# Optimization experiments

Hardware: AMD Instinct MI355X
Metric: run time of the kernel (lower is better)

Reference implementation:

```python
import jax, jax.numpy as jnp
import numpy as np

EPS = 1e-9
LDIM = 4  # dim_g + dim_t + dim_b + dim_w


def _mvn_logpdf(v, F):
    # batched zero-mean multivariate normal log-density, v: (N,O), F: (N,O,O)
    chol = jnp.linalg.cholesky(F)
    z = jax.scipy.linalg.solve_triangular(chol, v[..., None], lower=True)[..., 0]
    quad = jnp.sum(z * z, axis=-1)
    logdet = 2.0 * jnp.sum(jnp.log(jnp.diagonal(chol, axis1=-2, axis2=-1)), axis=-1)
    k = v.shape[-1]
    return -0.5 * (quad + logdet + k * jnp.log(2.0 * jnp.pi))


def _forward(y, B_G, B_T, B_B, B_W, lambda_r1_free, lambda_r2_free,
             q_diag, r_diag, gamma1, gamma2_learnable):
    N, Nt, O = y.shape
    L = LDIM
    # ----- _build_matrices -----
    B11 = jnp.zeros((L, L)).at[0, 0].set(B_G[0, 0]).at[1, 1].set(B_T[0, 0]).at[2, 2].set(B_B[0, 0])
    B22 = jnp.zeros((L, L)).at[3, 3].set(B_W[0, 0])
    B12 = jnp.zeros((L, L)).at[3, :3].set(1.0 / 3.0)  # regime1 factors feed shared factor
    B21 = jnp.zeros((L, L))
    L1 = jnp.zeros((O, L))
    L1 = L1.at[0, 0].set(1.0).at[1, 0].set(lambda_r1_free[0]).at[2, 0].set(lambda_r1_free[1])
    L1 = L1.at[3, 1].set(1.0).at[4, 1].set(lambda_r1_free[2]).at[5, 1].set(lambda_r1_free[3])
    L1 = L1.at[6, 2].set(1.0).at[7, 2].set(lambda_r1_free[4]).at[8, 2].set(lambda_r1_free[5])
    L2 = jnp.zeros((O, L)).at[0, 3].set(1.0).at[1:, 3].set(lambda_r2_free)
    Q = jnp.diag(jnp.abs(q_diag) + 1e-4)
    R = jnp.diag(jnp.abs(r_diag) + 1e-4)
    F_JIT = 1e-5 * jnp.eye(O)
    I_L = jnp.eye(L)
    P22_CONST = 0.9999

    # ----- initial beliefs ('informative') -----
    prob0 = jnp.tile(jnp.array([0.99, 0.01], jnp.float32), (N, 1))
    eta0 = jnp.zeros((N, L), y.dtype)
    P0 = jnp.tile(jnp.diag(jnp.array([1000.0, 1000.0, 1000.0, 1e-9], y.dtype))[None], (N, 1, 1))

    def predict(B, eta, P):
        # eta: (N,L), P: (N,L,L)
        return eta @ B.T, jnp.einsum('ij,njk,lk->nil', B, P, B) + Q

    def innov(Lm, e, Pp, y_t):
        v = y_t - e @ Lm.T
        F = jnp.einsum('oi,nij,pj->nop', Lm, Pp, Lm) + R + F_JIT
        return v, F

    def kupdate(e, Pp, Lm, v, F):
        LP = jnp.einsum('oi,nij->noj', Lm, Pp)          # (N,O,L)
        K = jnp.swapaxes(jnp.linalg.solve(F, LP), -1, -2)  # P Lm^T F^{-1}, (N,L,O)
        e_u = e + jnp.einsum('nlo,no->nl', K, v)
        IKL = I_L - K @ Lm                                # (N,L,L)
        P_u = IKL @ Pp @ jnp.swapaxes(IKL, -1, -2) + jnp.einsum('nlo,op,nmp->nlm', K, R, K)
        return e_u, P_u

    def collapse(w_a, w_b, e_a, e_b, P_a, P_b):
        e = w_a[:, None] * e_a + w_b[:, None] * e_b
        da, db = e_a - e, e_b - e
        P = (w_a[:, None, None] * (P_a + da[:, :, None] * da[:, None, :])
             + w_b[:, None, None] * (P_b + db[:, :, None] * db[:, None, :]))
        return e, P

    def step(carry, y_t):
        prob, eta1, eta2, P1, P2, ll = carry
        # HMM transition: p11 depends on regime-1 state (first L-1 components)
        logit_p11 = gamma1 + eta1[:, :3] @ gamma2_learnable
        p11 = jax.nn.sigmoid(logit_p11)
        # predictions for the 4 regime transitions (origin -> destination)
        e11, Pp11 = predict(B11, eta1, P1)
        e12, Pp12 = predict(B21, eta2, P2)
        e21, Pp21 = predict(B12, eta1, P1)
        e22, Pp22 = predict(B22, eta2, P2)
        v11, F11 = innov(L1, e11, Pp11, y_t)
        v12, F12 = innov(L1, e12, Pp12, y_t)
        v21, F21 = innov(L2, e21, Pp21, y_t)
        v22, F22 = innov(L2, e22, Pp22, y_t)
        ll11 = _mvn_logpdf(v11, F11)
        ll12 = _mvn_logpdf(v12, F12)
        ll21 = _mvn_logpdf(v21, F21)
        ll22 = _mvn_logpdf(v22, F22)
        lp = jnp.log(prob + EPS)
        c11 = lp[:, 0] + jnp.log(p11 + EPS) + ll11
        c12 = lp[:, 1] + np.log(1.0 - P22_CONST + EPS) + ll12
        c21 = lp[:, 0] + jnp.log(1.0 - p11 + EPS) + ll21
        c22 = lp[:, 1] + np.log(P22_CONST + EPS) + ll22
        logp = jnp.stack([c11, c12, c21, c22], axis=1)
        ll_t = jax.scipy.special.logsumexp(logp, axis=1)
        pt = jnp.exp(logp - ll_t[:, None])
        pr1 = pt[:, 0] + pt[:, 1]
        pr2 = pt[:, 2] + pt[:, 3]
        W11 = pt[:, 0] / (pr1 + EPS)
        W12 = pt[:, 1] / (pr1 + EPS)
        W21 = pt[:, 2] / (pr2 + EPS)
        W22 = pt[:, 3] / (pr2 + EPS)
        eu11, Pu11 = kupdate(e11, Pp11, L1, v11, F11)
        eu12, Pu12 = kupdate(e12, Pp12, L1, v12, F12)
        eu21, Pu21 = kupdate(e21, Pp21, L2, v21, F21)
        eu22, Pu22 = kupdate(e22, Pp22, L2, v22, F22)
        eta1n, P1n = collapse(W11, W12, eu11, eu12, Pu11, Pu12)
        eta2n, P2n = collapse(W21, W22, eu21, eu22, Pu21, Pu22)
        probn = jnp.stack([pr1, pr2], axis=1)
        return (probn, eta1n, eta2n, P1n, P2n, ll + ll_t.sum()), None

    carry0 = (prob0, eta0, eta0, P0, P0, jnp.zeros((), y.dtype))
    (_, _, _, _, _, total_ll), _ = jax.lax.scan(step, carry0, jnp.swapaxes(y, 0, 1))
    return total_ll


def setup_inputs() -> dict:
    key = jax.random.key(0)
    ks = jax.random.split(key, 12)
    N, Nt, O = 16384, 64, 9
    f32 = jnp.float32
    return {
        'y': jax.random.normal(ks[0], (N, Nt, O), f32),
        'B_G': jax.random.uniform(ks[1], (1, 1), f32, 0.6, 0.95),  # Beta(5,1.5)-like AR coeffs
        'B_T': jax.random.uniform(ks[2], (1, 1), f32, 0.6, 0.95),
        'B_B': jax.random.uniform(ks[3], (1, 1), f32, 0.6, 0.95),
        'B_W': jax.random.uniform(ks[4], (1, 1), f32, 0.6, 0.95),
        'lambda_r1_free': jax.random.normal(ks[5], (6,), f32),
        'lambda_r2_free': jax.random.normal(ks[6], (O - 1,), f32),
        'q_diag': jax.random.uniform(ks[7], (LDIM,), f32),
        'r_diag': jax.random.uniform(ks[8], (O,), f32),
        'gamma1': jnp.abs(jax.random.normal(ks[9], (), f32)),
        'gamma2_learnable': jax.random.normal(ks[10], (LDIM - 1,), f32),
    }


def reference(y, B_G, B_T, B_B, B_W, lambda_r1_free, lambda_r2_free,
              q_diag, r_diag, gamma1, gamma2_learnable):
    return _forward(y, B_G, B_T, B_B, B_W, lambda_r1_free, lambda_r2_free,
                    q_diag, r_diag, gamma1, gamma2_learnable)
```

## Files before the change

kernel.cpp:

```cpp
#include <hip/hip_runtime.h>


typedef float v2f __attribute__((ext_vector_type(2)));
typedef v2f v2fu __attribute__((aligned(4)));

static __device__ __forceinline__ float frcp(float x)  { return __builtin_amdgcn_rcpf(x); }
static __device__ __forceinline__ float frsq(float x)  { return __builtin_amdgcn_rsqf(x); }
static __device__ __forceinline__ float fexp2(float x) { return __builtin_amdgcn_exp2f(x); }
static __device__ __forceinline__ float flog2(float x) { return __builtin_amdgcn_logf(x); }
static __device__ __forceinline__ v2f sp(float x) { return (v2f){x, x}; }
static __device__ __forceinline__ v2f rsq2(v2f a) { return (v2f){frsq(a.x), frsq(a.y)}; }

#define EPSF   1e-9f
#define L2E    1.4426950408889634f
#define LN2    0.6931471805599453f
#define L2_2PI_9 23.86346461225016f
#define C12F   1.00001e-4f
#define P22F   0.99990001f
#define QK     (-0.5f * L2E)

__global__ __launch_bounds__(64, 1)
void kf_kernel(const float* __restrict__ y,
               const float* __restrict__ pBG, const float* __restrict__ pBT,
               const float* __restrict__ pBB, const float* __restrict__ pBW,
               const float* __restrict__ lam1, const float* __restrict__ lam2,
               const float* __restrict__ qd,  const float* __restrict__ rd,
               const float* __restrict__ pG1, const float* __restrict__ pG2,
               float* __restrict__ partial, int N, int Nt)
{
    const int lane = threadIdx.x;
    const int sid  = blockIdx.x * 64 + lane;
    const bool valid = (sid < N);
    const int rowlen = Nt * 9;

    const float bg = pBG[0], bt = pBT[0], bb = pBB[0], bw = pBW[0];
    const float a1 = lam1[0], a2 = lam1[1];
    const float a4 = lam1[2], a5 = lam1[3];
    const float a7 = lam1[4], a8 = lam1[5];
    float l2v[9], id[9], ld[9];
    l2v[0] = 1.f;
    #pragma unroll
    for (int i = 0; i < 8; ++i) l2v[i + 1] = lam2[i];
    float l2detD = 0.f;
    #pragma unroll
    for (int o = 0; o < 9; ++o) {
        float dv = fabsf(rd[o]) + 1.0e-4f + 1.0e-5f;
        id[o] = 1.0f / dv;
        ld[o] = l2v[o] * id[o];
        l2detD += flog2(dv);
    }
    const float id8 = id[8], ld8 = ld[8];
    const v2f idv01 = {id[0], id[1]}, idv23 = {id[2], id[3]},
              idv45 = {id[4], id[5]}, idv67 = {id[6], id[7]};
    const v2f ldv01 = {ld[0], ld[1]}, ldv23 = {ld[2], ld[3]},
              ldv45 = {ld[4], ld[5]}, ldv67 = {ld[6], ld[7]};
    const float aid0 = id[0],    aid1 = a1*id[1], aid2 = a2*id[2];
    const float aid3 = id[3],    aid4 = a4*id[4], aid5 = a5*id[5];
    const float aid6 = id[6],    aid7 = a7*id[7], aid8 = a8*id[8];
    const float q0 = fabsf(qd[0]) + 1e-4f, q1 = fabsf(qd[1]) + 1e-4f;
    const float q2 = fabsf(qd[2]) + 1e-4f, q3 = fabsf(qd[3]) + 1e-4f;
    const float g0 = id[0] + a1*a1*id[1] + a2*a2*id[2];
    const float g1 = id[3] + a4*a4*id[4] + a5*a5*id[5];
    const float g2 = id[6] + a7*a7*id[7] + a8*a8*id[8];
    float h = 0.f;
    #pragma unroll
    for (int o = 0; o < 9; ++o) h += l2v[o] * ld[o];
    const float pk0 = q0 / (1.f + q0 * g0);
    const float pk1 = q1 / (1.f + q1 * g1);
    const float pk2 = q2 / (1.f + q2 * g2);
    const float C12D = C12F * frsq((1.f + q0*g0) * (1.f + q1*g1) * (1.f + q2*g2));
    const float gam1 = pG1[0], w0c = pG2[0], w1c = pG2[1], w2c = pG2[2];
    const float CC = -0.5f * (l2detD + L2_2PI_9);
    const float bg2 = bg*bg, bt2 = bt*bt, bb2 = bb*bb, bw2 = bw*bw;
    const float bgbt = bg*bt, bgbb = bg*bb, btbb = bt*bb;
    const v2f hv = {h, h};

    float pf1 = 0.99f + EPSF, pf2 = 0.01f + EPSF;
    float se0 = 0.f, se1 = 0.f, se2 = 0.f;
    float p00 = 1000.f, p01 = 0.f, p02 = 0.f, p11 = 1000.f, p12 = 0.f, p22 = 1000.f;
    float sm2 = 0.f, sp2 = 1e-9f;
    float acc2 = 0.f;

    struct Yr { v2f ab, cd, ef, gh; float i8; };
    struct YB { float uy0, uy1, uy2, yl, ydy, f0, f1, f2, q12e; };

    const char* rowb = (const char*)(y + (size_t)(valid ? sid : 0) * rowlen);
    auto loadY = [&](Yr& r, int t) {
        const char* p = rowb + t * 36;
        r.ab = *(const v2fu*)(p);
        r.cd = *(const v2fu*)(p + 8);
        r.ef = *(const v2fu*)(p + 16);
        r.gh = *(const v2fu*)(p + 24);
        r.i8 = *(const float*)(p + 32);
    };
    auto computeYB = [&](const Yr& r) {
        YB o;
        v2f m0 = idv01*r.ab, m1 = idv23*r.cd, m2 = idv45*r.ef, m3 = idv67*r.gh;
        v2f yq = m0*r.ab + m1*r.cd + m2*r.ef + m3*r.gh;
        o.ydy = fmaf(id8*r.i8, r.i8, yq.x + yq.y);
        v2f la = ldv01*r.ab + ldv23*r.cd + ldv45*r.ef + ldv67*r.gh;
        o.yl = fmaf(ld8, r.i8, la.x + la.y);
        o.uy0 = fmaf(aid2, r.cd.x, fmaf(aid1, r.ab.y, aid0*r.ab.x));
        o.uy1 = fmaf(aid5, r.ef.y, fmaf(aid4, r.ef.x, aid3*r.cd.y));
        o.uy2 = fmaf(aid8, r.i8,   fmaf(aid7, r.gh.y, aid6*r.gh.x));
        o.f0 = pk0*o.uy0; o.f1 = pk1*o.uy1; o.f2 = pk2*o.uy2;
        o.q12e = QK * (o.ydy - (o.f0*o.uy0 + o.f1*o.uy1 + o.f2*o.uy2));
        return o;
    };

    auto step = [&](const YB& yb) {
        float logit = fmaf(w2c, se2, fmaf(w1c, se1, fmaf(w0c, se0, gam1)));
        float p11s = frcp(1.f + fexp2(-L2E * logit));
        float pp1 = pf1 * (p11s + EPSF);
        float pp2 = pf1 * (1.f - p11s + EPSF);

        float e0 = bg*se0, e1 = bt*se1, e2 = bb*se2;
        float s00 = fmaf(bg2, p00, q0), s11 = fmaf(bt2, p11, q1), s22 = fmaf(bb2, p22, q2);
        float s01 = bgbt*p01, s02 = bgbb*p02, s12 = btbb*p12;

        float u0 = fmaf(-g0, e0, yb.uy0);
        float u1 = fmaf(-g1, e1, yb.uy1);
        float u2 = fmaf(-g2, e2, yb.uy2);
        float vdv = yb.ydy - (e0*(yb.uy0+u0) + e1*(yb.uy1+u1) + e2*(yb.uy2+u2));

        float m00 = fmaf(s00, g0, 1.f), m11 = fmaf(s11, g1, 1.f), m22 = fmaf(s22, g2, 1.f);
        float m01 = s01*g1, m02 = s02*g2;
        float m10 = s01*g0, m20 = s02*g0;
        float m12 = s12*g2, m21 = s12*g1;
        float c00 = fmaf(m11, m22, -m12*m21);
        float c01 = fmaf(m12, m20, -m10*m22);
        float c02 = fmaf(m10, m21, -m11*m20);
        float c10 = fmaf(m02, m21, -m01*m22);
        float c11 = fmaf(m00, m22, -m02*m20);
        float c12 = fmaf(m01, m20, -m00*m21);
        float c20 = fmaf(m01, m12, -m02*m11);
        float c21 = fmaf(m02, m10, -m00*m12);
        float c22 = fmaf(m00, m11, -m01*m10);
        float det = fmaf(m02, c02, fmaf(m01, c01, m00*c00));
        float rs  = frsq(det);
        float iM  = rs * rs;
        float SC00 = fmaf(s02, c20, fmaf(s01, c10, s00*c00));
        float SC01 = fmaf(s02, c21, fmaf(s01, c11, s00*c01));
        float SC02 = fmaf(s02, c22, fmaf(s01, c12, s00*c02));
        float SC11 = fmaf(s12, c21, fmaf(s11, c11, s01*c01));
        float SC12 = fmaf(s12, c22, fmaf(s11, c12, s01*c02));
        float SC22 = fmaf(s22, c22, fmaf(s12, c12, s02*c02));

        float n0 = fmaf(SC02, u2, fmaf(SC01, u1, SC00*u0));
        float n1 = fmaf(SC12, u2, fmaf(SC11, u1, SC01*u0));
        float n2 = fmaf(SC22, u2, fmaf(SC12, u1, SC02*u0));
        float un = fmaf(u2, n2, fmaf(u1, n1, u0*n0));
        float quad11 = fmaf(-iM, un, vdv);
        float eu0 = fmaf(iM, n0, e0), eu1 = fmaf(iM, n1, e1), eu2 = fmaf(iM, n2, e2);

        float seS = se0 + se1 + se2;
        float sPs = fmaf(2.f, (p01 + p02) + p12, (p00 + p11) + p22);
        v2f m2v; m2v.x = seS * (1.f/3.f);          m2v.y = bw * sm2;
        v2f pvv; pvv.x = fmaf(sPs, 1.f/9.f, q3);   pvv.y = fmaf(bw2, sp2, q3);
        v2f ylv = sp(yb.yl);
        v2f u1v = ylv - m2v*hv;
        v2f vdav = sp(yb.ydy) - m2v*(sp(2.f*yb.yl) - m2v*hv);
        v2f denv = sp(1.f) + pvv*hv;
        v2f rv  = rsq2(denv);
        v2f puv = pvv*(rv*rv);
        v2f pu1 = puv*u1v;
        v2f quadv = vdav - pu1*u1v;
        v2f euv = m2v + pu1;

        float q11e = QK*quad11;
        float q21e = QK*quadv.x, q22e = QK*quadv.y;
        float Mq = fmaxf(fmaxf(q11e, yb.q12e), fmaxf(q21e, q22e));
        float w11 = pp1*rs        * fexp2(q11e - Mq);
        float w12 = pf2*C12D      * fexp2(yb.q12e - Mq);
        float w21 = pp2*rv.x      * fexp2(q21e - Mq);
        float w22 = pf2*P22F*rv.y * fexp2(q22e - Mq);
        float pr1n = w11 + w12, pr2n = w21 + w22;
        float ssum = pr1n + pr2n;
        acc2 += Mq + flog2(ssum);
        float inv1 = frcp(fmaf(EPSF, ssum, pr1n));
        float inv2 = frcp(fmaf(EPSF, ssum, pr2n));
        float issum = frcp(ssum);
        float W11 = w11*inv1, W12 = w12*inv1;
        float W21 = w21*inv2, W22 = w22*inv2;
        pf1 = fmaf(pr1n, issum, EPSF);
        pf2 = fmaf(pr2n, issum, EPSF);
        float W11i = W11 * iM;

        float ne0 = fmaf(W12, yb.f0, W11*eu0);
        float ne1 = fmaf(W12, yb.f1, W11*eu1);
        float ne2 = fmaf(W12, yb.f2, W11*eu2);
        float da0 = eu0-ne0, da1 = eu1-ne1, da2 = eu2-ne2;
        float db0 = yb.f0-ne0, db1 = yb.f1-ne1, db2 = yb.f2-ne2;
        p00 = fmaf(W12, fmaf(db0, db0, pk0), fmaf(W11, da0*da0, W11i*SC00));
        p01 = fmaf(W12, db0*db1,             fmaf(W11, da0*da1, W11i*SC01));
        p02 = fmaf(W12, db0*db2,             fmaf(W11, da0*da2, W11i*SC02));
        p11 = fmaf(W12, fmaf(db1, db1, pk1), fmaf(W11, da1*da1, W11i*SC11));
        p12 = fmaf(W12, db1*db2,             fmaf(W11, da1*da2, W11i*SC12));
        p22 = fmaf(W12, fmaf(db2, db2, pk2), fmaf(W11, da2*da2, W11i*SC22));
        se0 = ne0; se1 = ne1; se2 = ne2;

        float nm2 = fmaf(W22, euv.y, W21*euv.x);
        v2f dcv = euv - sp(nm2);
        v2f tv = puv + dcv*dcv;
        sp2 = fmaf(W22, tv.y, W21*tv.x);
        sm2 = nm2;
    };

    Yr A, B; YB ya, yb;
    loadY(A, 0);
    loadY(B, 1);
    ya = computeYB(A);
    for (int t = 0; t < Nt; t += 2) {
        step(ya);
        yb = computeYB(B);
        if (t + 2 < Nt) loadY(A, t + 2);
        step(yb);
        if (t + 2 < Nt) ya = computeYB(A);
        if (t + 3 < Nt) loadY(B, t + 3);
    }

    float acc = valid ? (acc2 + (float)Nt * CC) * LN2 : 0.f;
    #pragma unroll
    for (int off = 32; off; off >>= 1) acc += __shfl_down(acc, off, 64);
    if (lane == 0) partial[blockIdx.x] = acc;
}

__global__ __launch_bounds__(64)
void reduce_k(const float* __restrict__ part, float* __restrict__ out, int nb)
{
    float s = 0.f;
    for (int i = threadIdx.x; i < nb; i += 64) s += part[i];
    #pragma unroll
    for (int off = 32; off; off >>= 1) s += __shfl_down(s, off, 64);
    if (threadIdx.x == 0) out[0] = s;
}

extern "C" void kernel_launch(void* const* d_in, const int* in_sizes, int n_in,
                              void* d_out, int out_size, void* d_ws, size_t ws_size,
                              hipStream_t stream)
{
    const float* y    = (const float*)d_in[0];
    const float* pBG  = (const float*)d_in[1];
    const float* pBT  = (const float*)d_in[2];
    const float* pBB  = (const float*)d_in[3];
    const float* pBW  = (const float*)d_in[4];
    const float* lam1 = (const float*)d_in[5];
    const float* lam2 = (const float*)d_in[6];
    const float* qd   = (const float*)d_in[7];
    const float* rd   = (const float*)d_in[8];
    const float* pG1  = (const float*)d_in[9];
    const float* pG2  = (const float*)d_in[10];

    const int total = in_sizes[0];
    const int Nt = 64, O = 9;
    const int N = total / (Nt * O);
    const int blocks = (N + 63) / 64;

    float* partial = (float*)d_ws;
    kf_kernel<<<blocks, 64, 0, stream>>>(y, pBG, pBT, pBB, pBW, lam1, lam2,
                                         qd, rd, pG1, pG2, partial, N, Nt);
    reduce_k<<<1, 64, 0, stream>>>(partial, (float*)d_out, blocks);
}
```

Before: 127.6 us.

## Interleave two independent series per thread to raise instruction-level parallelism

```diff
diff --git a/kernel.cpp b/kernel.cpp
--- a/kernel.cpp
+++ b/kernel.cpp
@@ -29,8 +29,10 @@
                float* __restrict__ partial, int N, int Nt)
 {
     const int lane = threadIdx.x;
-    const int sid  = blockIdx.x * 64 + lane;
-    const bool valid = (sid < N);
+    const int base = blockIdx.x * 128;
+    const int sidA = base + lane;
+    const int sidB = base + 64 + lane;
+    const bool vA = (sidA < N), vB = (sidB < N);
     const int rowlen = Nt * 9;
 
     const float bg = pBG[0], bt = pBT[0], bb = pBB[0], bw = pBW[0];
@@ -75,17 +77,28 @@
     const float bgbt = bg*bt, bgbb = bg*bb, btbb = bt*bb;
     const v2f hv = {h, h};
 
-    float pf1 = 0.99f + EPSF, pf2 = 0.01f + EPSF;
-    float se0 = 0.f, se1 = 0.f, se2 = 0.f;
-    float p00 = 1000.f, p01 = 0.f, p02 = 0.f, p11 = 1000.f, p12 = 0.f, p22 = 1000.f;
-    float sm2 = 0.f, sp2 = 1e-9f;
-    float acc2 = 0.f;
+    struct St {
+        float pf1, pf2;
+        float se0, se1, se2;
+        float p00, p01, p02, p11, p12, p22;
+        float sm2, sp2, acc2;
+    };
+    auto initSt = [&](St& s) {
+        s.pf1 = 0.99f + EPSF; s.pf2 = 0.01f + EPSF;
+        s.se0 = 0.f; s.se1 = 0.f; s.se2 = 0.f;
+        s.p00 = 1000.f; s.p01 = 0.f; s.p02 = 0.f;
+        s.p11 = 1000.f; s.p12 = 0.f; s.p22 = 1000.f;
+        s.sm2 = 0.f; s.sp2 = 1e-9f; s.acc2 = 0.f;
+    };
+    St st0, st1;
+    initSt(st0); initSt(st1);
 
     struct Yr { v2f ab, cd, ef, gh; float i8; };
     struct YB { float uy0, uy1, uy2, yl, ydy, f0, f1, f2, q12e; };
 
-    const char* rowb = (const char*)(y + (size_t)(valid ? sid : 0) * rowlen);
-    auto loadY = [&](Yr& r, int t) {
+    const char* row0 = (const char*)(y + (size_t)(vA ? sidA : 0) * rowlen);
+    const char* row1 = (const char*)(y + (size_t)(vB ? sidB : 0) * rowlen);
+    auto loadY = [&](Yr& r, const char* rowb, int t) {
         const char* p = rowb + t * 36;
         r.ab = *(const v2fu*)(p);
         r.cd = *(const v2fu*)(p + 8);
@@ -108,15 +121,15 @@
         return o;
     };
 
-    auto step = [&](const YB& yb) {
-        float logit = fmaf(w2c, se2, fmaf(w1c, se1, fmaf(w0c, se0, gam1)));
+    auto step = [&](St& st, const YB& yb) {
+        float logit = fmaf(w2c, st.se2, fmaf(w1c, st.se1, fmaf(w0c, st.se0, gam1)));
         float p11s = frcp(1.f + fexp2(-L2E * logit));
-        float pp1 = pf1 * (p11s + EPSF);
-        float pp2 = pf1 * (1.f - p11s + EPSF);
-
-        float e0 = bg*se0, e1 = bt*se1, e2 = bb*se2;
-        float s00 = fmaf(bg2, p00, q0), s11 = fmaf(bt2, p11, q1), s22 = fmaf(bb2, p22, q2);
-        float s01 = bgbt*p01, s02 = bgbb*p02, s12 = btbb*p12;
+        float pp1 = st.pf1 * (p11s + EPSF);
+        float pp2 = st.pf1 * (1.f - p11s + EPSF);
+
+        float e0 = bg*st.se0, e1 = bt*st.se1, e2 = bb*st.se2;
+        float s00 = fmaf(bg2, st.p00, q0), s11 = fmaf(bt2, st.p11, q1), s22 = fmaf(bb2, st.p22, q2);
+        float s01 = bgbt*st.p01, s02 = bgbb*st.p02, s12 = btbb*st.p12;
 
         float u0 = fmaf(-g0, e0, yb.uy0);
         float u1 = fmaf(-g1, e1, yb.uy1);
@@ -153,10 +166,10 @@
         float quad11 = fmaf(-iM, un, vdv);
         float eu0 = fmaf(iM, n0, e0), eu1 = fmaf(iM, n1, e1), eu2 = fmaf(iM, n2, e2);
 
-        float seS = se0 + se1 + se2;
-        float sPs = fmaf(2.f, (p01 + p02) + p12, (p00 + p11) + p22);
-        v2f m2v; m2v.x = seS * (1.f/3.f);          m2v.y = bw * sm2;
-        v2f pvv; pvv.x = fmaf(sPs, 1.f/9.f, q3);   pvv.y = fmaf(bw2, sp2, q3);
+        float seS = st.se0 + st.se1 + st.se2;
+        float sPs = fmaf(2.f, (st.p01 + st.p02) + st.p12, (st.p00 + st.p11) + st.p22);
+        v2f m2v; m2v.x = seS * (1.f/3.f);          m2v.y = bw * st.sm2;
+        v2f pvv; pvv.x = fmaf(sPs, 1.f/9.f, q3);   pvv.y = fmaf(bw2, st.sp2, q3);
         v2f ylv = sp(yb.yl);
         v2f u1v = ylv - m2v*hv;
         v2f vdav = sp(yb.ydy) - m2v*(sp(2.f*yb.yl) - m2v*hv);
@@ -170,20 +183,20 @@
         float q11e = QK*quad11;
         float q21e = QK*quadv.x, q22e = QK*quadv.y;
         float Mq = fmaxf(fmaxf(q11e, yb.q12e), fmaxf(q21e, q22e));
-        float w11 = pp1*rs        * fexp2(q11e - Mq);
-        float w12 = pf2*C12D      * fexp2(yb.q12e - Mq);
-        float w21 = pp2*rv.x      * fexp2(q21e - Mq);
-        float w22 = pf2*P22F*rv.y * fexp2(q22e - Mq);
+        float w11 = pp1*rs           * fexp2(q11e - Mq);
+        float w12 = st.pf2*C12D      * fexp2(yb.q12e - Mq);
+        float w21 = pp2*rv.x         * fexp2(q21e - Mq);
+        float w22 = st.pf2*P22F*rv.y * fexp2(q22e - Mq);
         float pr1n = w11 + w12, pr2n = w21 + w22;
         float ssum = pr1n + pr2n;
-        acc2 += Mq + flog2(ssum);
+        st.acc2 += Mq + flog2(ssum);
         float inv1 = frcp(fmaf(EPSF, ssum, pr1n));
         float inv2 = frcp(fmaf(EPSF, ssum, pr2n));
         float issum = frcp(ssum);
         float W11 = w11*inv1, W12 = w12*inv1;
         float W21 = w21*inv2, W22 = w22*inv2;
-        pf1 = fmaf(pr1n, issum, EPSF);
-        pf2 = fmaf(pr2n, issum, EPSF);
+        st.pf1 = fmaf(pr1n, issum, EPSF);
+        st.pf2 = fmaf(pr2n, issum, EPSF);
         float W11i = W11 * iM;
 
         float ne0 = fmaf(W12, yb.f0, W11*eu0);
@@ -191,35 +204,39 @@
         float ne2 = fmaf(W12, yb.f2, W11*eu2);
         float da0 = eu0-ne0, da1 = eu1-ne1, da2 = eu2-ne2;
         float db0 = yb.f0-ne0, db1 = yb.f1-ne1, db2 = yb.f2-ne2;
-        p00 = fmaf(W12, fmaf(db0, db0, pk0), fmaf(W11, da0*da0, W11i*SC00));
-        p01 = fmaf(W12, db0*db1,             fmaf(W11, da0*da1, W11i*SC01));
-        p02 = fmaf(W12, db0*db2,             fmaf(W11, da0*da2, W11i*SC02));
-        p11 = fmaf(W12, fmaf(db1, db1, pk1), fmaf(W11, da1*da1, W11i*SC11));
-        p12 = fmaf(W12, db1*db2,             fmaf(W11, da1*da2, W11i*SC12));
-        p22 = fmaf(W12, fmaf(db2, db2, pk2), fmaf(W11, da2*da2, W11i*SC22));
-        se0 = ne0; se1 = ne1; se2 = ne2;
+        st.p00 = fmaf(W12, fmaf(db0, db0, pk0), fmaf(W11, da0*da0, W11i*SC00));
+        st.p01 = fmaf(W12, db0*db1,             fmaf(W11, da0*da1, W11i*SC01));
+        st.p02 = fmaf(W12, db0*db2,             fmaf(W11, da0*da2, W11i*SC02));
+        st.p11 = fmaf(W12, fmaf(db1, db1, pk1), fmaf(W11, da1*da1, W11i*SC11));
+        st.p12 = fmaf(W12, db1*db2,             fmaf(W11, da1*da2, W11i*SC12));
+        st.p22 = fmaf(W12, fmaf(db2, db2, pk2), fmaf(W11, da2*da2, W11i*SC22));
+        st.se0 = ne0; st.se1 = ne1; st.se2 = ne2;
 
         float nm2 = fmaf(W22, euv.y, W21*euv.x);
         v2f dcv = euv - sp(nm2);
         v2f tv = puv + dcv*dcv;
-        sp2 = fmaf(W22, tv.y, W21*tv.x);
-        sm2 = nm2;
-    };
-
-    Yr A, B; YB ya, yb;
-    loadY(A, 0);
-    loadY(B, 1);
-    ya = computeYB(A);
+        st.sp2 = fmaf(W22, tv.y, W21*tv.x);
+        st.sm2 = nm2;
+    };
+
+    Yr A0, B0, A1, B1; YB ya0, yb0, ya1, yb1;
+    loadY(A0, row0, 0); loadY(A1, row1, 0);
+    loadY(B0, row0, 1); loadY(B1, row1, 1);
+    ya0 = computeYB(A0); ya1 = computeYB(A1);
     for (int t = 0; t < Nt; t += 2) {
-        step(ya);
-        yb = computeYB(B);
-        if (t + 2 < Nt) loadY(A, t + 2);
-        step(yb);
-        if (t + 2 < Nt) ya = computeYB(A);
-        if (t + 3 < Nt) loadY(B, t + 3);
+        step(st0, ya0);
+        step(st1, ya1);
+        yb0 = computeYB(B0); yb1 = computeYB(B1);
+        if (t + 2 < Nt) { loadY(A0, row0, t + 2); loadY(A1, row1, t + 2); }
+        step(st0, yb0);
+        step(st1, yb1);
+        if (t + 2 < Nt) { ya0 = computeYB(A0); ya1 = computeYB(A1); }
+        if (t + 3 < Nt) { loadY(B0, row0, t + 3); loadY(B1, row1, t + 3); }
     }
 
-    float acc = valid ? (acc2 + (float)Nt * CC) * LN2 : 0.f;
+    float acc = 0.f;
+    if (vA) acc += (st0.acc2 + (float)Nt * CC) * LN2;
+    if (vB) acc += (st1.acc2 + (float)Nt * CC) * LN2;
     #pragma unroll
     for (int off = 32; off; off >>= 1) acc += __shfl_down(acc, off, 64);
     if (lane == 0) partial[blockIdx.x] = acc;
@@ -254,7 +271,7 @@
     const int total = in_sizes[0];
     const int Nt = 64, O = 9;
     const int N = total / (Nt * O);
-    const int blocks = (N + 63) / 64;
+    const int blocks = (N + 127) / 128;
 
     float* partial = (float*)d_ws;
     kf_kernel<<<blocks, 64, 0, stream>>>(y, pBG, pBT, pBB, pBW, lam1, lam2,
```

New measurement: 160.2 us. 25.5% more time.
